# Performance work log

Measured on AMD Instinct MI355X. Metric: run time of the kernel, lower is better.

The kernel has to match this reference:

```python
import jax, jax.numpy as jnp
import numpy as np

N_HEAD, D_MODEL, D_K, D_V = 16, 1024, 64, 64
B, S = 4, 2048
LN_EPS = 1e-5

def setup_inputs() -> dict:
    key = jax.random.key(0)
    ks = jax.random.split(key, 12)
    s = 1.0 / np.sqrt(D_MODEL)
    x = jax.random.normal(ks[0], (B, S, D_MODEL), dtype=jnp.float32)
    Wq = jax.random.normal(ks[1], (N_HEAD, D_MODEL, D_K), dtype=jnp.float32) * s
    bq = jax.random.normal(ks[2], (N_HEAD, D_K), dtype=jnp.float32) * 0.01
    Wk = jax.random.normal(ks[3], (N_HEAD, D_MODEL, D_K), dtype=jnp.float32) * s
    bk = jax.random.normal(ks[4], (N_HEAD, D_K), dtype=jnp.float32) * 0.01
    Wv = jax.random.normal(ks[5], (N_HEAD, D_MODEL, D_V), dtype=jnp.float32) * s
    bv = jax.random.normal(ks[6], (N_HEAD, D_V), dtype=jnp.float32) * 0.01
    Wfc = jax.random.normal(ks[7], (N_HEAD * D_V, D_MODEL), dtype=jnp.float32) * (1.0 / np.sqrt(N_HEAD * D_V))
    bfc = jax.random.normal(ks[8], (D_MODEL,), dtype=jnp.float32) * 0.01
    gamma = jnp.ones((D_MODEL,), dtype=jnp.float32)
    beta = jnp.zeros((D_MODEL,), dtype=jnp.float32)
    return {"x": x, "Wq": Wq, "bq": bq, "Wk": Wk, "bk": bk, "Wv": Wv, "bv": bv,
            "Wfc": Wfc, "bfc": bfc, "gamma": gamma, "beta": beta}

def reference(x, Wq, bq, Wk, bk, Wv, bv, Wfc, bfc, gamma, beta):
    # Per-head projections batched over heads: [B,H,S,d]
    q = jnp.einsum('bsd,hdk->bhsk', x, Wq) + bq[None, :, None, :]
    k = jnp.einsum('bsd,hdk->bhsk', x, Wk) + bk[None, :, None, :]
    v = jnp.einsum('bsd,hdv->bhsv', x, Wv) + bv[None, :, None, :]
    scores = jnp.einsum('bhqk,bhsk->bhqs', q, k) / jnp.sqrt(jnp.float32(D_K))
    probs = jax.nn.softmax(scores, axis=-1)
    attn = jnp.einsum('bhqs,bhsv->bhqv', probs, v)  # [B,H,S,Dv]
    # concat heads (cat along last dim == transpose heads to feature axis)
    cat = attn.transpose(0, 2, 1, 3).reshape(B, S, N_HEAD * D_V)
    y = cat @ Wfc + bfc
    mu = jnp.mean(y, axis=-1, keepdims=True)
    var = jnp.mean(jnp.square(y - mu), axis=-1, keepdims=True)
    return (y - mu) * jax.lax.rsqrt(var + LN_EPS) * gamma + beta
```

## Files before the change

### kernel.cpp

```cpp
#include <hip/hip_runtime.h>

#define NH 16
#define DMODEL 1024
#define DK 64
#define DV 64
#define BB 4
#define SS 2048
#define NTOK (BB*SS)
#define LN_EPS 1e-5f
#define SM_SHIFT 13.0f

typedef __attribute__((ext_vector_type(4))) float f32x4;
typedef __attribute__((ext_vector_type(8))) short s16x8;
typedef __attribute__((ext_vector_type(4))) short s16x4;

__device__ __forceinline__ short f2bf(float f) {
    union { float f; unsigned u; } a; a.f = f;
    unsigned r = a.u + 0x7FFFu + ((a.u >> 16) & 1u);
    return (short)(r >> 16);
}
__device__ __forceinline__ unsigned pk2(float a, float b) {
    union { float f; unsigned u; } x, y; x.f = a; y.f = b;
    return __builtin_amdgcn_perm(x.u + 0x8000u, y.u + 0x8000u, 0x07060302u);
}
__device__ __forceinline__ float fexp2(float x) { return __builtin_amdgcn_exp2f(x); }
__device__ __forceinline__ void gll16(const void* g, void* l) {
    __builtin_amdgcn_global_load_lds(
        (const __attribute__((address_space(1))) unsigned int*)g,
        (__attribute__((address_space(3))) unsigned int*)l, 16, 0, 0);
}

__global__ void k_cast_x(const float* __restrict__ x, short* __restrict__ xb) {
    int i = blockIdx.x * blockDim.x + threadIdx.x;
    f32x4 v = reinterpret_cast<const f32x4*>(x)[i];
    s16x4 o;
    o[0] = f2bf(v[0]); o[1] = f2bf(v[1]); o[2] = f2bf(v[2]); o[3] = f2bf(v[3]);
    reinterpret_cast<s16x4*>(xb)[i] = o;
}

__global__ __launch_bounds__(256) void k_conv_wqkv_t(const float* __restrict__ Wq,
                                                     const float* __restrict__ Wk,
                                                     const float* __restrict__ Wv,
                                                     short* __restrict__ WT) {
    __shared__ float tile[64][17];
    const int mh = blockIdx.y;
    const int mat = mh >> 4, h = mh & 15;
    const int dt = blockIdx.x >> 2, kt = blockIdx.x & 3;
    const float* src = (mat == 0 ? Wq : (mat == 1 ? Wk : Wv));
    const int t = threadIdx.x;
    #pragma unroll
    for (int p = 0; p < 4; p++) {
        int d = p * 16 + (t >> 4), kk = t & 15;
        tile[d][kk] = src[((size_t)h * 1024 + dt * 64 + d) * 64 + kt * 16 + kk];
    }
    __syncthreads();
    #pragma unroll
    for (int p = 0; p < 4; p++) {
        int kk = p * 4 + (t >> 6), d = t & 63;
        WT[((size_t)mat * 1024 + h * 64 + kt * 16 + kk) * 1024 + dt * 64 + d] = f2bf(tile[d][kk]);
    }
}

__global__ __launch_bounds__(256) void k_conv_wfc_t(const float* __restrict__ Wfc,
                                                    short* __restrict__ WfcT) {
    __shared__ float tile[64][17];
    const int ct = blockIdx.x >> 6, nt = blockIdx.x & 63;
    const int t = threadIdx.x;
    #pragma unroll
    for (int p = 0; p < 4; p++) {
        int c = p * 16 + (t >> 4), n = t & 15;
        tile[c][n] = Wfc[((size_t)ct * 64 + c) * 1024 + nt * 16 + n];
    }
    __syncthreads();
    #pragma unroll
    for (int p = 0; p < 4; p++) {
        int n = p * 4 + (t >> 6), c = t & 63;
        WfcT[((size_t)nt * 16 + n) * 1024 + ct * 64 + c] = f2bf(tile[c][n]);
    }
}

template<int MODE, int NBX, int NWG>
__global__ __launch_bounds__(256) void k_gemm2(const short* __restrict__ A,
                                               const short* __restrict__ BT,
                                               const float* __restrict__ bq,
                                               const float* __restrict__ bk,
                                               const float* __restrict__ bv,
                                               const float* __restrict__ bfc,
                                               short* __restrict__ Qb,
                                               short* __restrict__ Kb,
                                               short* __restrict__ Vb,
                                               short* __restrict__ Yb) {
    __shared__ short smem[2][128][64];
    const int fid = blockIdx.x + blockIdx.y * NBX;
    const int swzid = (fid & 7) * (NWG / 8) + (fid >> 3);
    const int gm0 = (swzid / NBX) * 128, gn0 = (swzid % NBX) * 128;
    const int t = threadIdx.x, lane = t & 63, w = t >> 6;
    const int wm = w >> 1, wn = w & 1;
    const int lr = lane & 15, lg = lane >> 4;

    f32x4 acc[4][4] = {};

    const int lrow = t >> 3, gl = t & 7;
    const int sgx = (gl ^ (lrow & 7)) << 3;
    const short* pa = A  + (size_t)(gm0 + lrow) * 1024 + sgx;
    const short* pb = BT + (size_t)(gn0 + lrow) * 1024 + sgx;
    char* dA = (char*)smem[0] + w * 1024;
    char* dB = (char*)smem[1] + w * 1024;

    const int x7 = lr & 7;
    const int gx0 = (lg ^ x7) << 4;
    const int gx1 = ((4 + lg) ^ x7) << 4;

    for (int k0 = 0; k0 < 1024; k0 += 64) {
        #pragma unroll
        for (int c = 0; c < 4; c++) {
            gll16(pa + (size_t)c * 32768 + k0, dA + c * 4096);
            gll16(pb + (size_t)c * 32768 + k0, dB + c * 4096);
        }
        __syncthreads();
        s16x8 aF[2][4], bF[2][4];
        #pragma unroll
        for (int i = 0; i < 4; i++) {
            const char* rpa = (char*)smem[0] + (wm * 64 + i * 16 + lr) * 128;
            const char* rpb = (char*)smem[1] + (wn * 64 + i * 16 + lr) * 128;
            aF[0][i] = *(const s16x8*)(rpa + gx0);
            aF[1][i] = *(const s16x8*)(rpa + gx1);
            bF[0][i] = *(const s16x8*)(rpb + gx0);
            bF[1][i] = *(const s16x8*)(rpb + gx1);
        }
        __builtin_amdgcn_s_setprio(1);
        #pragma unroll
        for (int kk = 0; kk < 2; kk++)
            #pragma unroll
            for (int i = 0; i < 4; i++)
                #pragma unroll
                for (int j = 0; j < 4; j++)
                    acc[i][j] = __builtin_amdgcn_mfma_f32_16x16x32_bf16(aF[kk][i], bF[kk][j], acc[i][j], 0, 0, 0);
        __builtin_amdgcn_s_setprio(0);
        __syncthreads();
    }

    short (*ct)[128] = (short(*)[128])smem;
    const float* bias; int nloc0; float scale = 1.0f;
    if (MODE == 0) {
        if (gn0 < 1024)      { bias = bq; nloc0 = gn0;        scale = 0.18033688011112042f; }
        else if (gn0 < 2048) { bias = bk; nloc0 = gn0 - 1024; }
        else                 { bias = bv; nloc0 = gn0 - 2048; }
    } else { bias = bfc; nloc0 = gn0; }
    float bval[4];
    #pragma unroll
    for (int j = 0; j < 4; j++) bval[j] = bias[nloc0 + wn * 64 + j * 16 + lr];

    #pragma unroll
    for (int i = 0; i < 4; i++)
        #pragma unroll
        for (int j = 0; j < 4; j++) {
            const int colg = wn * 4 + j;
            #pragma unroll
            for (int rg = 0; rg < 4; rg++) {
                int row = wm * 64 + i * 16 + lg * 4 + rg;
                int cg = colg ^ ((row >> 1) & 7);
                ct[row][(cg << 4) + lr] = f2bf((acc[i][j][rg] + bval[j]) * scale);
            }
        }
    __syncthreads();

    short* dstM = (MODE == 0) ? (gn0 < 1024 ? Qb : (gn0 < 2048 ? Kb : Vb)) : Yb;
    #pragma unroll
    for (int rr = 0; rr < 2; rr++) {
        const int row = w * 16 + (lane >> 2) + rr * 64;
        const int m = gm0 + row;
        const int swz = (row >> 1) & 7;
        #pragma unroll
        for (int j = 0; j < 4; j++) {
            const int c = (lane & 3) + j * 4;
            const int cg = (c >> 1) ^ swz;
            s16x8 v = *(const s16x8*)((char*)ct + row * 256 + (cg << 5) + (c & 1) * 16);
            if (MODE == 0) {
                int b2 = m >> 11, s2 = m & 2047;
                int n0 = (gn0 & 1023) + c * 8;
                int h2 = n0 >> 6, kk = n0 & 63;
                *(s16x8*)(dstM + ((size_t)(b2 * NH + h2) * SS + s2) * DK + kk) = v;
            } else {
                *(s16x8*)(dstM + (size_t)m * 1024 + gn0 + c * 8) = v;
            }
        }
    }
}

__global__ __launch_bounds__(256) void k_transpose_v(const short* __restrict__ Vb,
                                                     short* __restrict__ VT) {
    __shared__ short tile[64][65];
    const int bh = blockIdx.y, s0 = blockIdx.x * 64;
    const short* src = Vb + ((size_t)bh * SS + s0) * 64;
    short* dst = VT + (size_t)bh * 64 * SS;
    const int t = threadIdx.x;
    {
        int r = t >> 2, c0 = (t & 3) * 16;
        s16x8 v0 = *reinterpret_cast<const s16x8*>(&src[r * 64 + c0]);
        s16x8 v1 = *reinterpret_cast<const s16x8*>(&src[r * 64 + c0 + 8]);
        #pragma unroll
        for (int i = 0; i < 8; i++) { tile[r][c0 + i] = v0[i]; tile[r][c0 + 8 + i] = v1[i]; }
    }
    __syncthreads();
    {
        int vv = t >> 2, so = (t & 3) * 16;
        int b32 = so >> 5, half = (so >> 4) & 1;
        short* drow = dst + (size_t)vv * SS + s0 + b32 * 32 + half * 4;
        #pragma unroll
        for (int lgp = 0; lgp < 4; lgp++) {
            s16x4 c;
            #pragma unroll
            for (int i = 0; i < 4; i++) c[i] = tile[b32 * 32 + half * 16 + lgp * 4 + i][vv];
            *reinterpret_cast<s16x4*>(drow + lgp * 8) = c;
        }
    }
}

__global__ __launch_bounds__(256) void k_attn2(const short* __restrict__ Qb,
                                               const short* __restrict__ Kb,
                                               const short* __restrict__ VT2,
                                               short* __restrict__ cat) {
    __shared__ char smem[2][16384];
    const int fid = blockIdx.x + blockIdx.y * gridDim.x;
    const int swz = ((fid & 7) << 7) | (fid >> 3);
    const int qt = swz & 15, bh = swz >> 4;
    const int b = bh >> 4, h = bh & 15;
    const int t = threadIdx.x, lane = t & 63, w = t >> 6;
    const int lr = lane & 15, lg = lane >> 4;

    const short* Qbase = Qb + ((size_t)bh * SS + qt * 128 + w * 32) * DK;
    s16x8 qF[2][2];
    #pragma unroll
    for (int f = 0; f < 2; f++) {
        qF[f][0] = *(const s16x8*)(Qbase + (f * 16 + lr) * DK + lg * 8);
        qF[f][1] = *(const s16x8*)(Qbase + (f * 16 + lr) * DK + 32 + lg * 8);
    }
    s16x8 onesF;
    #pragma unroll
    for (int i = 0; i < 8; i++) onesF[i] = (short)0x3F80;

    const char* Kbase = (const char*)(Kb + (size_t)bh * SS * DK);
    const char* Vbase = (const char*)(VT2 + (size_t)bh * DK * SS);
    const int rk0 = w * 16 + (lane >> 3), rk1 = rk0 + 8;
    const int gl = lane & 7;
    const char* pK0 = Kbase + rk0 * 128 + ((gl ^ (rk0 & 7)) << 4);
    const char* pK1 = Kbase + rk1 * 128 + ((gl ^ (rk1 & 7)) << 4);
    const char* pV0 = Vbase + rk0 * (SS * 2) + ((gl ^ (rk0 & 7)) << 4);
    const char* pV1 = Vbase + rk1 * (SS * 2) + ((gl ^ (rk1 & 7)) << 4);

    const int x7 = lr & 7;
    const int gx0 = (lg ^ x7) << 4;
    const int gx1 = ((4 + lg) ^ x7) << 4;

    f32x4 acc[2][4] = {};
    f32x4 accs[2] = {};
    const f32x4 zinit = {-SM_SHIFT, -SM_SHIFT, -SM_SHIFT, -SM_SHIFT};

    {
        char* d = smem[0];
        gll16(pK0, d + w * 2048);
        gll16(pK1, d + w * 2048 + 1024);
        gll16(pV0, d + 8192 + w * 2048);
        gll16(pV1, d + 8192 + w * 2048 + 1024);
    }
    __syncthreads();

    int cur = 0;
    for (int kt = 0; kt < SS; kt += 64) {
        if (kt + 64 < SS) {
            char* d = smem[cur ^ 1];
            const int oK = (kt + 64) * 128, oV = (kt + 64) * 2;
            gll16(pK0 + oK, d + w * 2048);
            gll16(pK1 + oK, d + w * 2048 + 1024);
            gll16(pV0 + oV, d + 8192 + w * 2048);
            gll16(pV1 + oV, d + 8192 + w * 2048 + 1024);
        }
        const char* bs = smem[cur];

        s16x8 kA[4][2];
        #pragma unroll
        for (int kg = 0; kg < 4; kg++) {
            const char* rp = bs + (kg * 16 + lr) * 128;
            kA[kg][0] = *(const s16x8*)(rp + gx0);
            kA[kg][1] = *(const s16x8*)(rp + gx1);
        }
        f32x4 st[2][4];
        __builtin_amdgcn_s_setprio(1);
        #pragma unroll
        for (int f = 0; f < 2; f++)
            #pragma unroll
            for (int kg = 0; kg < 4; kg++) {
                f32x4 z = __builtin_amdgcn_mfma_f32_16x16x32_bf16(kA[kg][0], qF[f][0], zinit, 0, 0, 0);
                st[f][kg] = __builtin_amdgcn_mfma_f32_16x16x32_bf16(kA[kg][1], qF[f][1], z, 0, 0, 0);
            }
        __builtin_amdgcn_s_setprio(0);

        s16x8 pb[2][2];
        #pragma unroll
        for (int f = 0; f < 2; f++) {
            float p[4][4];
            #pragma unroll
            for (int kg = 0; kg < 4; kg++)
                #pragma unroll
                for (int rg = 0; rg < 4; rg++)
                    p[kg][rg] = fexp2(st[f][kg][rg]);
            #pragma unroll
            for (int ks = 0; ks < 2; ks++) {
                union { s16x8 v; unsigned u[4]; } U;
                U.u[0] = pk2(p[2 * ks][1],     p[2 * ks][0]);
                U.u[1] = pk2(p[2 * ks][3],     p[2 * ks][2]);
                U.u[2] = pk2(p[2 * ks + 1][1], p[2 * ks + 1][0]);
                U.u[3] = pk2(p[2 * ks + 1][3], p[2 * ks + 1][2]);
                pb[f][ks] = U.v;
            }
        }

        __builtin_amdgcn_s_setprio(1);
        #pragma unroll
        for (int f = 0; f < 2; f++) {
            accs[f] = __builtin_amdgcn_mfma_f32_16x16x32_bf16(onesF, pb[f][0], accs[f], 0, 0, 0);
            accs[f] = __builtin_amdgcn_mfma_f32_16x16x32_bf16(onesF, pb[f][1], accs[f], 0, 0, 0);
        }
        #pragma unroll
        for (int vt = 0; vt < 4; vt++) {
            const char* rp = bs + 8192 + (vt * 16 + lr) * 128;
            s16x8 vA0 = *(const s16x8*)(rp + gx0);
            s16x8 vA1 = *(const s16x8*)(rp + gx1);
            #pragma unroll
            for (int f = 0; f < 2; f++) {
                acc[f][vt] = __builtin_amdgcn_mfma_f32_16x16x32_bf16(vA0, pb[f][0], acc[f][vt], 0, 0, 0);
                acc[f][vt] = __builtin_amdgcn_mfma_f32_16x16x32_bf16(vA1, pb[f][1], acc[f][vt], 0, 0, 0);
            }
        }
        __builtin_amdgcn_s_setprio(0);
        __syncthreads();
        cur ^= 1;
    }

    char* ods = smem[0] + w * 4096;
    float inv[2] = {1.0f / accs[0][0], 1.0f / accs[1][0]};
    #pragma unroll
    for (int f = 0; f < 2; f++)
        #pragma unroll
        for (int vt = 0; vt < 4; vt++)
            #pragma unroll
            for (int rg = 0; rg < 4; rg++)
                *(short*)(ods + (f * 16 + lr) * 128 + (vt * 16 + lg * 4 + rg) * 2) =
                    f2bf(acc[f][vt][rg] * inv[f]);
    __syncthreads();
    {
        int r = lane >> 1, hb = lane & 1;
        const char* srow = smem[0] + w * 4096 + r * 128 + hb * 64;
        int token = b * SS + qt * 128 + w * 32 + r;
        char* dst = (char*)(cat + (size_t)token * 1024 + h * 64 + hb * 32);
        #pragma unroll
        for (int i = 0; i < 4; i++)
            *(s16x8*)(dst + i * 16) = *(const s16x8*)(srow + i * 16);
    }
}

__global__ __launch_bounds__(256) void k_ln(const short* __restrict__ Yb,
                                            const float* __restrict__ gamma,
                                            const float* __restrict__ beta,
                                            float* __restrict__ out) {
    const int row = blockIdx.x;
    const int t = threadIdx.x;
    s16x4 raw = reinterpret_cast<const s16x4*>(Yb + (size_t)row * 1024)[t];
    float v[4];
    #pragma unroll
    for (int i = 0; i < 4; i++) {
        union { unsigned u; float f; } cvt;
        cvt.u = ((unsigned)(unsigned short)raw[i]) << 16;
        v[i] = cvt.f;
    }
    float s = v[0] + v[1] + v[2] + v[3];
    float s2 = v[0] * v[0] + v[1] * v[1] + v[2] * v[2] + v[3] * v[3];
    #pragma unroll
    for (int off = 32; off; off >>= 1) {
        s += __shfl_xor(s, off);
        s2 += __shfl_xor(s2, off);
    }
    __shared__ float red[8];
    int w = t >> 6, lane = t & 63;
    if (lane == 0) { red[w] = s; red[4 + w] = s2; }
    __syncthreads();
    float S = red[0] + red[1] + red[2] + red[3];
    float S2 = red[4] + red[5] + red[6] + red[7];
    float mu = S * (1.f / 1024.f);
    float var = S2 * (1.f / 1024.f) - mu * mu;
    float rs = rsqrtf(var + LN_EPS);
    f32x4 g = reinterpret_cast<const f32x4*>(gamma)[t];
    f32x4 be = reinterpret_cast<const f32x4*>(beta)[t];
    f32x4 o;
    #pragma unroll
    for (int i = 0; i < 4; i++) o[i] = (v[i] - mu) * rs * g[i] + be[i];
    reinterpret_cast<f32x4*>(out + (size_t)row * 1024)[t] = o;
}

extern "C" void kernel_launch(void* const* d_in, const int* in_sizes, int n_in,
                              void* d_out, int out_size, void* d_ws, size_t ws_size,
                              hipStream_t stream) {
    const float* x    = (const float*)d_in[0];
    const float* Wq   = (const float*)d_in[1];
    const float* bq   = (const float*)d_in[2];
    const float* Wk   = (const float*)d_in[3];
    const float* bk   = (const float*)d_in[4];
    const float* Wv   = (const float*)d_in[5];
    const float* bv   = (const float*)d_in[6];
    const float* Wfc  = (const float*)d_in[7];
    const float* bfc  = (const float*)d_in[8];
    const float* gamma= (const float*)d_in[9];
    const float* beta = (const float*)d_in[10];
    float* out = (float*)d_out;

    char* p = (char*)d_ws;
    short* xb   = (short*)p; p += (size_t)NTOK * 1024 * 2;
    short* WT   = (short*)p; p += (size_t)3072 * 1024 * 2;
    short* WfcT = (short*)p; p += (size_t)1024 * 1024 * 2;
    short* Qb   = (short*)p; p += (size_t)64 * SS * 64 * 2;
    short* Kb   = (short*)p; p += (size_t)64 * SS * 64 * 2;
    short* Vb   = (short*)p; p += (size_t)64 * SS * 64 * 2;
    short* VTb  = (short*)p; p += (size_t)64 * 64 * SS * 2;
    short* cat  = (short*)p; p += (size_t)NTOK * 1024 * 2;
    short* Yb   = Qb;

    k_cast_x     <<<NTOK * 1024 / 4 / 256, 256, 0, stream>>>(x, xb);
    k_conv_wqkv_t<<<dim3(64, 48), 256, 0, stream>>>(Wq, Wk, Wv, WT);
    k_conv_wfc_t <<<1024, 256, 0, stream>>>(Wfc, WfcT);
    k_gemm2<0, 24, 1536><<<dim3(24, 64), 256, 0, stream>>>(xb, WT, bq, bk, bv, nullptr, Qb, Kb, Vb, nullptr);
    k_transpose_v<<<dim3(SS / 64, 64), 256, 0, stream>>>(Vb, VTb);
    k_attn2      <<<dim3(16, 64), 256, 0, stream>>>(Qb, Kb, VTb, cat);
    k_gemm2<1, 8, 512><<<dim3(8, 64), 256, 0, stream>>>(cat, WfcT, nullptr, nullptr, nullptr, bfc, nullptr, nullptr, nullptr, Yb);
    k_ln         <<<NTOK, 256, 0, stream>>>(Yb, gamma, beta, out);
}
```

Measured before the change: 204.0 us.

## Load V fragments directly from global into registers, drop V LDS staging

The attention kernel no longer stages V tiles through LDS. Each lane loads its V MFMA operand fragments directly from global memory at the top of each key tile, and LDS shrinks to double-buffered K only. This removes the LDS writes and reads for V and halves shared memory per block, which may allow more blocks per CU, but it exposes global-load latency inside the loop with no prefetch. The bf16 packing of probabilities also switches from round-to-nearest to truncation to save two adds per pair, at a small cost in precision.

```diff
diff --git a/kernel.cpp b/kernel.cpp
--- a/kernel.cpp
+++ b/kernel.cpp
@@ -19,9 +19,9 @@
     unsigned r = a.u + 0x7FFFu + ((a.u >> 16) & 1u);
     return (short)(r >> 16);
 }
-__device__ __forceinline__ unsigned pk2(float a, float b) {
+__device__ __forceinline__ unsigned pk2t(float a, float b) {
     union { float f; unsigned u; } x, y; x.f = a; y.f = b;
-    return __builtin_amdgcn_perm(x.u + 0x8000u, y.u + 0x8000u, 0x07060302u);
+    return __builtin_amdgcn_perm(x.u, y.u, 0x07060302u);
 }
 __device__ __forceinline__ float fexp2(float x) { return __builtin_amdgcn_exp2f(x); }
 __device__ __forceinline__ void gll16(const void* g, void* l) {
@@ -221,7 +221,7 @@
                                                const short* __restrict__ Kb,
                                                const short* __restrict__ VT2,
                                                short* __restrict__ cat) {
-    __shared__ char smem[2][16384];
+    __shared__ char smem[2][8192];
     const int fid = blockIdx.x + blockIdx.y * gridDim.x;
     const int swz = ((fid & 7) << 7) | (fid >> 3);
     const int qt = swz & 15, bh = swz >> 4;
@@ -246,8 +246,9 @@
     const int gl = lane & 7;
     const char* pK0 = Kbase + rk0 * 128 + ((gl ^ (rk0 & 7)) << 4);
     const char* pK1 = Kbase + rk1 * 128 + ((gl ^ (rk1 & 7)) << 4);
-    const char* pV0 = Vbase + rk0 * (SS * 2) + ((gl ^ (rk0 & 7)) << 4);
-    const char* pV1 = Vbase + rk1 * (SS * 2) + ((gl ^ (rk1 & 7)) << 4);
+    const char* pVr[4];
+    #pragma unroll
+    for (int vt = 0; vt < 4; vt++) pVr[vt] = Vbase + (size_t)(vt * 16 + lr) * (SS * 2);
 
     const int x7 = lr & 7;
     const int gx0 = (lg ^ x7) << 4;
@@ -261,8 +262,6 @@
         char* d = smem[0];
         gll16(pK0, d + w * 2048);
         gll16(pK1, d + w * 2048 + 1024);
-        gll16(pV0, d + 8192 + w * 2048);
-        gll16(pV1, d + 8192 + w * 2048 + 1024);
     }
     __syncthreads();
 
@@ -270,13 +269,18 @@
     for (int kt = 0; kt < SS; kt += 64) {
         if (kt + 64 < SS) {
             char* d = smem[cur ^ 1];
-            const int oK = (kt + 64) * 128, oV = (kt + 64) * 2;
+            const int oK = (kt + 64) * 128;
             gll16(pK0 + oK, d + w * 2048);
             gll16(pK1 + oK, d + w * 2048 + 1024);
-            gll16(pV0 + oV, d + 8192 + w * 2048);
-            gll16(pV1 + oV, d + 8192 + w * 2048 + 1024);
         }
         const char* bs = smem[cur];
+
+        s16x8 vA[4][2];
+        #pragma unroll
+        for (int vt = 0; vt < 4; vt++) {
+            vA[vt][0] = *(const s16x8*)(pVr[vt] + kt * 2 + lg * 16);
+            vA[vt][1] = *(const s16x8*)(pVr[vt] + kt * 2 + (4 + lg) * 16);
+        }
 
         s16x8 kA[4][2];
         #pragma unroll
@@ -308,10 +312,10 @@
             #pragma unroll
             for (int ks = 0; ks < 2; ks++) {
                 union { s16x8 v; unsigned u[4]; } U;
-                U.u[0] = pk2(p[2 * ks][1],     p[2 * ks][0]);
-                U.u[1] = pk2(p[2 * ks][3],     p[2 * ks][2]);
-                U.u[2] = pk2(p[2 * ks + 1][1], p[2 * ks + 1][0]);
-                U.u[3] = pk2(p[2 * ks + 1][3], p[2 * ks + 1][2]);
+                U.u[0] = pk2t(p[2 * ks][1],     p[2 * ks][0]);
+                U.u[1] = pk2t(p[2 * ks][3],     p[2 * ks][2]);
+                U.u[2] = pk2t(p[2 * ks + 1][1], p[2 * ks + 1][0]);
+                U.u[3] = pk2t(p[2 * ks + 1][3], p[2 * ks + 1][2]);
                 pb[f][ks] = U.v;
             }
         }
@@ -323,22 +327,18 @@
             accs[f] = __builtin_amdgcn_mfma_f32_16x16x32_bf16(onesF, pb[f][1], accs[f], 0, 0, 0);
         }
         #pragma unroll
-        for (int vt = 0; vt < 4; vt++) {
-            const char* rp = bs + 8192 + (vt * 16 + lr) * 128;
-            s16x8 vA0 = *(const s16x8*)(rp + gx0);
-            s16x8 vA1 = *(const s16x8*)(rp + gx1);
+        for (int vt = 0; vt < 4; vt++)
             #pragma unroll
             for (int f = 0; f < 2; f++) {
-                acc[f][vt] = __builtin_amdgcn_mfma_f32_16x16x32_bf16(vA0, pb[f][0], acc[f][vt], 0, 0, 0);
-                acc[f][vt] = __builtin_amdgcn_mfma_f32_16x16x32_bf16(vA1, pb[f][1], acc[f][vt], 0, 0, 0);
+                acc[f][vt] = __builtin_amdgcn_mfma_f32_16x16x32_bf16(vA[vt][0], pb[f][0], acc[f][vt], 0, 0, 0);
+                acc[f][vt] = __builtin_amdgcn_mfma_f32_16x16x32_bf16(vA[vt][1], pb[f][1], acc[f][vt], 0, 0, 0);
             }
-        }
         __builtin_amdgcn_s_setprio(0);
         __syncthreads();
         cur ^= 1;
     }
 
-    char* ods = smem[0] + w * 4096;
+    char* ods = (char*)smem + w * 4096;
     float inv[2] = {1.0f / accs[0][0], 1.0f / accs[1][0]};
     #pragma unroll
     for (int f = 0; f < 2; f++)
@@ -351,7 +351,7 @@
     __syncthreads();
     {
         int r = lane >> 1, hb = lane & 1;
-        const char* srow = smem[0] + w * 4096 + r * 128 + hb * 64;
+        const char* srow = (char*)smem + w * 4096 + r * 128 + hb * 64;
         int token = b * SS + qt * 128 + w * 32 + r;
         char* dst = (char*)(cat + (size_t)token * 1024 + h * 64 + hb * 32);
         #pragma unroll
```

New measurement: 258.8 us. 26.9% more time.
